# Kernel tuning notes

Hardware: AMD Instinct MI355X
Metric: run time of the kernel (lower is better)

Reference implementation:

```python
import jax, jax.numpy as jnp
import numpy as np

N_NODES = 100000
NUM_FEATURES = 512
HIDDEN = 64
NUM_CLASSES = 40
N_EDGES = 3200000
K = 10
ALPHA = 0.1


def setup_inputs() -> dict:
    key = jax.random.key(0)
    ks = jax.random.split(key, 7)
    x = jax.random.normal(ks[0], (N_NODES, NUM_FEATURES), dtype=jnp.float32)
    edge_index = jax.random.randint(ks[1], (2, N_EDGES), 0, N_NODES, dtype=jnp.int64)
    # linear layers (PyTorch Linear default init ~ U(-1/sqrt(fan_in), 1/sqrt(fan_in)))
    b1lim = 1.0 / np.sqrt(NUM_FEATURES)
    w1 = jax.random.uniform(ks[2], (NUM_FEATURES, HIDDEN), jnp.float32, -b1lim, b1lim)
    b1 = jax.random.uniform(ks[3], (HIDDEN,), jnp.float32, -b1lim, b1lim)
    b2lim = 1.0 / np.sqrt(HIDDEN)
    w2 = jax.random.uniform(ks[4], (HIDDEN, NUM_CLASSES), jnp.float32, -b2lim, b2lim)
    b2 = jax.random.uniform(ks[5], (NUM_CLASSES,), jnp.float32, -b2lim, b2lim)
    # PPR init of GPR gamma coefficients: alpha*(1-alpha)^k, last = (1-alpha)^K
    temp = ALPHA * (1.0 - ALPHA) ** np.arange(K + 1)
    temp[-1] = (1.0 - ALPHA) ** K
    temp = jnp.asarray(temp, dtype=jnp.float32)
    return {"x": x, "edge_index": edge_index, "w1": w1, "b1": b1,
            "w2": w2, "b2": b2, "temp": temp}


def reference(x, edge_index, w1, b1, w2, b2, temp):
    n = x.shape[0]
    # MLP (eval mode: dropout is identity)
    h = jax.nn.relu(x @ w1 + b1)
    h = h @ w2 + b2  # [N, C]

    gamma = jax.nn.relu(temp)

    # gcn_norm with self-loops (edge_weight = 1)
    loop = jnp.arange(n, dtype=edge_index.dtype)
    src = jnp.concatenate([edge_index[0], loop])
    dst = jnp.concatenate([edge_index[1], loop])
    ew = jnp.ones(src.shape[0], dtype=h.dtype)
    deg = jax.ops.segment_sum(ew, dst, num_segments=n)
    dinv = jnp.where(deg > 0, jax.lax.rsqrt(deg), 0.0)
    norm = dinv[src] * ew * dinv[dst]  # [E+N]

    # K-step gamma-weighted propagation: out = sum_k gamma_k * A_hat^k h
    out = gamma[0] * h
    cur = h
    for k in range(K):
        cur = jax.ops.segment_sum(norm[:, None] * cur[src], dst, num_segments=n)
        out = out + gamma[k + 1] * cur
    return jax.nn.log_softmax(out, axis=1)
```

## Files before the change

kernel.cpp:

```cpp
#include <hip/hip_runtime.h>
#include <hip/hip_bf16.h>
#include <hip/hip_fp16.h>
#include <hip/hip_fp8.h>

#define NFEAT 512
#define HID   64
#define NCLS  40

typedef short bf16x8 __attribute__((ext_vector_type(8)));
typedef float f32x4  __attribute__((ext_vector_type(4)));
typedef float v2f    __attribute__((ext_vector_type(2)));

__device__ inline short bfs(float f) {
  __hip_bfloat16 h = __float2bfloat16(f);
  return __builtin_bit_cast(short, h);
}
__device__ inline int pk(float a, float b) {
  return (int)(unsigned short)bfs(a) | ((int)(unsigned short)bfs(b) << 16);
}

__device__ inline v2f cvt2lo(int v) {
#if __has_builtin(__builtin_amdgcn_cvt_pk_f32_fp8)
  return __builtin_amdgcn_cvt_pk_f32_fp8(v, false);
#else
  v2f r; const unsigned char* b = (const unsigned char*)&v;
  __hip_fp8_e4m3 h0; h0.__x = b[0]; r[0] = (float)h0;
  __hip_fp8_e4m3 h1; h1.__x = b[1]; r[1] = (float)h1;
  return r;
#endif
}
__device__ inline v2f cvt2hi(int v) {
#if __has_builtin(__builtin_amdgcn_cvt_pk_f32_fp8)
  return __builtin_amdgcn_cvt_pk_f32_fp8(v, true);
#else
  v2f r; const unsigned char* b = (const unsigned char*)&v;
  __hip_fp8_e4m3 h0; h0.__x = b[2]; r[0] = (float)h0;
  __hip_fp8_e4m3 h1; h1.__x = b[3]; r[1] = (float)h1;
  return r;
#endif
}
__device__ inline int2 pk8f8(const float f[8]) {
#if __has_builtin(__builtin_amdgcn_cvt_pk_fp8_f32)
  int lo = 0, hi = 0;
  lo = __builtin_amdgcn_cvt_pk_fp8_f32(f[0], f[1], lo, false);
  lo = __builtin_amdgcn_cvt_pk_fp8_f32(f[2], f[3], lo, true);
  hi = __builtin_amdgcn_cvt_pk_fp8_f32(f[4], f[5], hi, false);
  hi = __builtin_amdgcn_cvt_pk_fp8_f32(f[6], f[7], hi, true);
  return make_int2(lo, hi);
#else
  int2 r; unsigned char* b = (unsigned char*)&r;
  #pragma unroll
  for (int i = 0; i < 8; ++i) { __hip_fp8_e4m3 h((float)f[i]); b[i] = h.__x; }
  return r;
#endif
}
__device__ inline unsigned char f8b(float v) {
#if __has_builtin(__builtin_amdgcn_cvt_pk_fp8_f32)
  int r = __builtin_amdgcn_cvt_pk_fp8_f32(v, v, 0, false);
  return (unsigned char)(r & 0xff);
#else
  __hip_fp8_e4m3 h(v); return h.__x;
#endif
}


static __global__ void deg_i_kernel(const int* __restrict__ dst, int* __restrict__ deg, int E) {
  int e = blockIdx.x * blockDim.x + threadIdx.x;
  if (e < E) atomicAdd(&deg[dst[e]], 1);
}

static __global__ void dinv_kernel(const int* __restrict__ deg, float* __restrict__ dinv, int N) {
  int i = blockIdx.x * blockDim.x + threadIdx.x;
  if (i < N) dinv[i] = rsqrtf((float)deg[i] + 1.0f);
}

static __global__ void w1conv_kernel(const float* __restrict__ w1, short* __restrict__ w1bf,
                                     int* __restrict__ bcnt, int nbz) {
  int t = blockIdx.x * blockDim.x + threadIdx.x;
  if (t < nbz) bcnt[t] = 0;
  if (t >= NFEAT * HID) return;
  int k = t >> 6, n = t & 63;
  w1bf[n * NFEAT + k] = bfs(w1[k * HID + n]);
}
static __global__ void w2conv_kernel(const float* __restrict__ w2, short* __restrict__ w2bf) {
  int t = blockIdx.x * blockDim.x + threadIdx.x;
  if (t >= 48 * HID) return;
  int n = t >> 6, k = t & 63;
  w2bf[t] = (n < NCLS) ? bfs(w2[k * NCLS + n]) : (short)0;
}

static __global__ __launch_bounds__(256) void mlp_mfma_kernel(
    const float* __restrict__ x, const short* __restrict__ w1bf, const float* __restrict__ b1,
    const short* __restrict__ w2bf, const float* __restrict__ b2, const float* __restrict__ temp,
    const float* __restrict__ dinv, unsigned char* __restrict__ cur, float* __restrict__ out, int N)
{
  __shared__ __align__(16) short Al[64][72];
  __shared__ __align__(16) short Bl[64][72];
  __shared__ __align__(16) short Hl[64][72];
  __shared__ __align__(16) short W2l[48][72];
  const int tid = threadIdx.x;
  const int w = tid >> 6, lane = tid & 63;
  const int q = lane >> 4, m = lane & 15;
  const long row0 = (long)blockIdx.x * 64;

  if (tid < 192) {
    int n = tid >> 2, ch = tid & 3;
    const int4* sp = (const int4*)(w2bf + n * 64 + ch * 16);
    *(int4*)&W2l[n][ch * 16]     = sp[0];
    *(int4*)&W2l[n][ch * 16 + 8] = sp[1];
  }

  f32x4 zf = {0.f, 0.f, 0.f, 0.f};
  f32x4 acc[4] = {zf, zf, zf, zf};

  const int ar = tid >> 2, ch = tid & 3;
  const long gr = row0 + ar;

  for (int kk = 0; kk < NFEAT; kk += 64) {
    float4 v0, v1, v2, v3;
    if (gr < N) {
      const float4* xp = (const float4*)(x + gr * NFEAT + kk + ch * 16);
      v0 = xp[0]; v1 = xp[1]; v2 = xp[2]; v3 = xp[3];
    } else {
      v0 = v1 = v2 = v3 = make_float4(0.f, 0.f, 0.f, 0.f);
    }
    const int4* bp = (const int4*)(w1bf + ar * NFEAT + kk + ch * 16);
    int4 bv0 = bp[0], bv1 = bp[1];

    __syncthreads();
    int4 a0 = make_int4(pk(v0.x, v0.y), pk(v0.z, v0.w), pk(v1.x, v1.y), pk(v1.z, v1.w));
    int4 a1 = make_int4(pk(v2.x, v2.y), pk(v2.z, v2.w), pk(v3.x, v3.y), pk(v3.z, v3.w));
    *(int4*)&Al[ar][ch * 16]     = a0;
    *(int4*)&Al[ar][ch * 16 + 8] = a1;
    *(int4*)&Bl[ar][ch * 16]     = bv0;
    *(int4*)&Bl[ar][ch * 16 + 8] = bv1;
    __syncthreads();

    #pragma unroll
    for (int s = 0; s < 2; ++s) {
      bf16x8 a = *(const bf16x8*)&Al[w * 16 + m][s * 32 + q * 8];
      #pragma unroll
      for (int c = 0; c < 4; ++c) {
        bf16x8 b = *(const bf16x8*)&Bl[c * 16 + m][s * 32 + q * 8];
        acc[c] = __builtin_amdgcn_mfma_f32_16x16x32_bf16(a, b, acc[c], 0, 0, 0);
      }
    }
  }

  #pragma unroll
  for (int c = 0; c < 4; ++c) {
    int col = c * 16 + m;
    float bb = b1[col];
    #pragma unroll
    for (int r = 0; r < 4; ++r) {
      int rl = w * 16 + q * 4 + r;
      Hl[rl][col] = bfs(fmaxf(acc[c][r] + bb, 0.0f));
    }
  }
  __syncthreads();

  f32x4 acc2[3] = {zf, zf, zf};
  #pragma unroll
  for (int s = 0; s < 2; ++s) {
    bf16x8 a = *(const bf16x8*)&Hl[w * 16 + m][s * 32 + q * 8];
    #pragma unroll
    for (int c = 0; c < 3; ++c) {
      bf16x8 b = *(const bf16x8*)&W2l[c * 16 + m][s * 32 + q * 8];
      acc2[c] = __builtin_amdgcn_mfma_f32_16x16x32_bf16(a, b, acc2[c], 0, 0, 0);
    }
  }

  float g0 = fmaxf(temp[0], 0.0f);
  #pragma unroll
  for (int c = 0; c < 3; ++c) {
    int col = c * 16 + m;
    if (col < NCLS) {
      float bb = b2[col];
      #pragma unroll
      for (int r = 0; r < 4; ++r) {
        long grow = row0 + w * 16 + q * 4 + r;
        if (grow < N) {
          float vv = acc2[c][r] + bb;
          cur[grow * 64 + col] = f8b(dinv[grow] * vv);
          out[grow * NCLS + col] = g0 * vv;
        }
      }
    }
  }
}


static __global__ __launch_bounds__(256) void scan1_kernel(const int* __restrict__ deg,
                                                           int* __restrict__ bsum, int N) {
  __shared__ int s[256];
  int tid = threadIdx.x;
  int i = blockIdx.x * 256 + tid;
  s[tid] = (i < N) ? deg[i] : 0;
  __syncthreads();
  for (int off = 128; off > 0; off >>= 1) {
    if (tid < off) s[tid] += s[tid + off];
    __syncthreads();
  }
  if (tid == 0) bsum[blockIdx.x] = s[0];
}

static __global__ __launch_bounds__(512) void scan2_kernel(int* __restrict__ bsum,
                                                           int* __restrict__ total, int nb) {
  __shared__ int s[512];
  int tid = threadIdx.x;
  int v = (tid < nb) ? bsum[tid] : 0;
  s[tid] = v;
  __syncthreads();
  for (int off = 1; off < 512; off <<= 1) {
    int t = (tid >= off) ? s[tid - off] : 0;
    __syncthreads();
    s[tid] += t;
    __syncthreads();
  }
  if (tid < nb) bsum[tid] = s[tid] - v;
  if (tid == 511) *total = s[511];
}

static __global__ __launch_bounds__(256) void scan3_kernel(const int* __restrict__ deg,
                                                           const int* __restrict__ bsum,
                                                           const int* __restrict__ total,
                                                           int* __restrict__ rowptr,
                                                           int* __restrict__ cursor, int N) {
  __shared__ int s[256];
  int tid = threadIdx.x;
  int i = blockIdx.x * 256 + tid;
  int v = (i < N) ? deg[i] : 0;
  s[tid] = v;
  __syncthreads();
  for (int off = 1; off < 256; off <<= 1) {
    int t = (tid >= off) ? s[tid - off] : 0;
    __syncthreads();
    s[tid] += t;
    __syncthreads();
  }
  if (i < N) {
    int e = bsum[blockIdx.x] + s[tid] - v;
    rowptr[i] = e;
    cursor[i] = e;
  }
  if (i == N) rowptr[N] = *total;
}


#define FB_EPT 16
#define FB_EPB (256 * FB_EPT)
#define FB_NBMAX 512
#define FS_CAP 12288

static __global__ __launch_bounds__(256) void bcount_kernel(
    const int* __restrict__ dst, int* __restrict__ bcnt, int E, int NB)
{
  __shared__ int cnt[FB_NBMAX];
  const int tid = threadIdx.x;
  cnt[tid] = 0; cnt[tid + 256] = 0;
  __syncthreads();
  const int e0 = blockIdx.x * FB_EPB;
  #pragma unroll
  for (int j = 0; j < FB_EPT; ++j) {
    int e = e0 + j * 256 + tid;
    if (e < E) atomicAdd(&cnt[dst[e] >> 8], 1);
  }
  __syncthreads();
  int b0 = tid, b1 = tid + 256;
  if (b0 < NB && cnt[b0]) atomicAdd(&bcnt[b0], cnt[b0]);
  if (b1 < NB && cnt[b1]) atomicAdd(&bcnt[b1], cnt[b1]);
}

static __global__ __launch_bounds__(512) void bscan_kernel(
    const int* __restrict__ bcnt, int* __restrict__ bbase, int* __restrict__ bcur,
    int* __restrict__ rowptr, int NB, int N, int E)
{
  __shared__ int s[512];
  int tid = threadIdx.x;
  int v = (tid < NB) ? bcnt[tid] : 0;
  s[tid] = v;
  __syncthreads();
  for (int off = 1; off < 512; off <<= 1) {
    int t = (tid >= off) ? s[tid - off] : 0;
    __syncthreads();
    s[tid] += t;
    __syncthreads();
  }
  if (tid < NB) { int ex = s[tid] - v; bbase[tid] = ex; bcur[tid] = ex; }
  if (tid == 0) rowptr[N] = E;
}

static __global__ __launch_bounds__(256) void fill_bin_kernel(
    const int* __restrict__ src, const int* __restrict__ dst,
    int* __restrict__ bcur, int* __restrict__ csr, int E, int NB)
{
  __shared__ int cnt[FB_NBMAX];
  __shared__ int pfx[FB_NBMAX];
  __shared__ int gbase[FB_NBMAX];
  __shared__ int stg[FB_EPB];
  __shared__ unsigned short bmap[FB_EPB];
  const int tid = threadIdx.x;
  const int e0 = blockIdx.x * FB_EPB;

  cnt[tid] = 0; cnt[tid + 256] = 0;
  __syncthreads();

  int pk_[FB_EPT], b_[FB_EPT], r_[FB_EPT];
  #pragma unroll
  for (int j = 0; j < FB_EPT; ++j) {
    int e = e0 + j * 256 + tid;
    if (e < E) {
      int s = src[e], d = dst[e];
      pk_[j] = s | ((d & 255) << 17);
      b_[j] = d >> 8;
      r_[j] = atomicAdd(&cnt[b_[j]], 1);
    } else b_[j] = -1;
  }
  __syncthreads();

  pfx[tid] = cnt[tid]; pfx[tid + 256] = cnt[tid + 256];
  __syncthreads();
  for (int off = 1; off < FB_NBMAX; off <<= 1) {
    int a = (tid >= off) ? pfx[tid - off] : 0;
    int b = (tid + 256 >= off) ? pfx[tid + 256 - off] : 0;
    __syncthreads();
    pfx[tid] += a; pfx[tid + 256] += b;
    __syncthreads();
  }

  {
    int b0 = tid, b1 = tid + 256;
    if (b0 < NB && cnt[b0]) gbase[b0] = atomicAdd(&bcur[b0], cnt[b0]);
    if (b1 < NB && cnt[b1]) gbase[b1] = atomicAdd(&bcur[b1], cnt[b1]);
  }
  __syncthreads();

  #pragma unroll
  for (int j = 0; j < FB_EPT; ++j) {
    if (b_[j] >= 0) {
      int slot = pfx[b_[j]] - cnt[b_[j]] + r_[j];
      stg[slot] = pk_[j];
      bmap[slot] = (unsigned short)b_[j];
    }
  }
  __syncthreads();

  const int total = pfx[FB_NBMAX - 1];
  for (int slot = tid; slot < total; slot += 256) {
    int b = bmap[slot];
    int local = slot - (pfx[b] - cnt[b]);
    csr[gbase[b] + local] = stg[slot];
  }
}

static __global__ __launch_bounds__(256) void fill_scatter2_kernel(
    const int* __restrict__ bbase_a, const int* __restrict__ bcnt,
    int* __restrict__ csr, const int* __restrict__ src, const int* __restrict__ dst,
    float* __restrict__ dinv, int* __restrict__ rowptr, int N, int E)
{
  __shared__ int degl[256];
  __shared__ int pfx[256];
  __shared__ int curl[256];
  __shared__ int buf[FS_CAP];
  const int tid = threadIdx.x;
  const int b = blockIdx.x;
  const int base = bbase_a[b], cnt = bcnt[b];
  const int node = (b << 8) + tid;

  degl[tid] = 0;
  __syncthreads();
  if (cnt <= FS_CAP) {
    for (int i = tid; i < cnt; i += 256) {
      int p = csr[base + i];
      atomicAdd(&degl[(p >> 17) & 255], 1);
    }
  } else {
    for (int e = tid; e < E; e += 256) {
      int d = dst[e];
      if ((d >> 8) == b) atomicAdd(&degl[d & 255], 1);
    }
  }
  __syncthreads();
  const int dv = degl[tid];
  if (node < N) dinv[node] = rsqrtf((float)dv + 1.0f);

  pfx[tid] = dv;
  __syncthreads();
  for (int off = 1; off < 256; off <<= 1) {
    int t = (tid >= off) ? pfx[tid - off] : 0;
    __syncthreads();
    pfx[tid] += t;
    __syncthreads();
  }
  const int ex = pfx[tid] - dv;
  if (node < N) rowptr[node] = base + ex;
  curl[tid] = ex;
  __syncthreads();

  if (cnt <= FS_CAP) {
    for (int i = tid; i < cnt; i += 256) {
      int p = csr[base + i];
      int ld = (p >> 17) & 255;
      int pos = atomicAdd(&curl[ld], 1);
      buf[pos] = p & 0x1FFFF;
    }
    __syncthreads();
    for (int i = tid; i < cnt; i += 256) csr[base + i] = buf[i];
  } else {
    curl[tid] = base + ex;
    __syncthreads();
    for (int e = tid; e < E; e += 256) {
      int d = dst[e];
      if ((d >> 8) == b) {
        int pos = atomicAdd(&curl[d & 255], 1);
        csr[pos] = src[e];
      }
    }
  }
}


static __global__ void fill_kernel(const int* __restrict__ src, const int* __restrict__ dst,
                                   int* __restrict__ cursor, int* __restrict__ csr, int E) {
  int e = blockIdx.x * blockDim.x + threadIdx.x;
  if (e >= E) return;
  int s = src[e], d = dst[e];
  int pos = atomicAdd(&cursor[d], 1);
  csr[pos] = s;
}


#define GR_ROWS 51
#define GR_CAP  2560

template <bool INLDS>
__device__ inline void gather_row(
    const int* __restrict__ ip, int beg, int end, unsigned c8,
    const unsigned char* __restrict__ cur,
    v2f& a0, v2f& a1, v2f& a2, v2f& a3)
{
  int e = beg;
  for (; e + 7 < end; e += 8) {
    int idx[8];
    #pragma unroll
    for (int j = 0; j < 8; ++j) idx[j] = ip[e + j];
    int2 g[8];
    #pragma unroll
    for (int j = 0; j < 8; ++j) g[j] = *(const int2*)(cur + (((unsigned)idx[j] << 6) | c8));
    #pragma unroll
    for (int j = 0; j < 8; ++j) {
      a0 += cvt2lo(g[j].x); a1 += cvt2hi(g[j].x);
      a2 += cvt2lo(g[j].y); a3 += cvt2hi(g[j].y);
    }
  }
  for (; e + 3 < end; e += 4) {
    int idx[4];
    #pragma unroll
    for (int j = 0; j < 4; ++j) idx[j] = ip[e + j];
    int2 g[4];
    #pragma unroll
    for (int j = 0; j < 4; ++j) g[j] = *(const int2*)(cur + (((unsigned)idx[j] << 6) | c8));
    #pragma unroll
    for (int j = 0; j < 4; ++j) {
      a0 += cvt2lo(g[j].x); a1 += cvt2hi(g[j].x);
      a2 += cvt2lo(g[j].y); a3 += cvt2hi(g[j].y);
    }
  }
  for (; e < end; ++e) {
    int2 g = *(const int2*)(cur + (((unsigned)ip[e] << 6) | c8));
    a0 += cvt2lo(g.x); a1 += cvt2hi(g.x);
    a2 += cvt2lo(g.y); a3 += cvt2hi(g.y);
  }
}

static __global__ __launch_bounds__(256) void gather_kernel(
    const int* __restrict__ rowptr, const int* __restrict__ csr,
    const float* __restrict__ dinv, const float* __restrict__ temp, int k,
    const unsigned char* __restrict__ cur, unsigned char* __restrict__ nxt,
    float4* __restrict__ out, int N)
{
  __shared__ int rp[GR_ROWS + 1];
  __shared__ int lidx[GR_CAP];
  const int tid = threadIdx.x;
  const int row0 = blockIdx.x * GR_ROWS;
  const int nrows = min(GR_ROWS, N - row0);

  if (tid <= nrows) rp[tid] = rowptr[row0 + tid];
  __syncthreads();
  const int beg0 = rp[0];
  const int count = rp[nrows] - beg0;
  const bool inlds = (count <= GR_CAP);
  if (inlds) {
    for (int i = tid; i < count; i += 256) lidx[i] = csr[beg0 + i];
  }
  __syncthreads();

  const int r = tid / 5, c4 = tid - r * 5;
  if (r >= nrows) return;
  const int row = row0 + r;
  const unsigned c8 = (unsigned)c4 * 8;
  const float dv = dinv[row];

  v2f a0, a1, a2, a3;
  {
    int2 v = *(const int2*)(cur + (((unsigned)row << 6) | c8));
    a0 = cvt2lo(v.x); a1 = cvt2hi(v.x);
    a2 = cvt2lo(v.y); a3 = cvt2hi(v.y);
  }

  if (inlds) {
    gather_row<true>(lidx, rp[r] - beg0, rp[r + 1] - beg0, c8, cur, a0, a1, a2, a3);
  } else {
    gather_row<false>(csr, rp[r], rp[r + 1], c8, cur, a0, a1, a2, a3);
  }

  float d2 = dv * dv;
  float y[8] = {d2 * a0[0], d2 * a0[1], d2 * a1[0], d2 * a1[1],
                d2 * a2[0], d2 * a2[1], d2 * a3[0], d2 * a3[1]};
  *(int2*)(nxt + (((unsigned)row << 6) | c8)) = pk8f8(y);

  float gd = fmaxf(temp[k], 0.0f) * dv;
  int oi = row * 10 + c4 * 2;
  float4 o0 = out[oi], o1 = out[oi + 1];
  out[oi]     = make_float4(fmaf(gd, a0[0], o0.x), fmaf(gd, a0[1], o0.y),
                            fmaf(gd, a1[0], o0.z), fmaf(gd, a1[1], o0.w));
  out[oi + 1] = make_float4(fmaf(gd, a2[0], o1.x), fmaf(gd, a2[1], o1.y),
                            fmaf(gd, a3[0], o1.z), fmaf(gd, a3[1], o1.w));
}


static __global__ void selfloop_kernel(const float* __restrict__ dinv, const float4* __restrict__ cur,
                                       float4* __restrict__ nxt, int n10) {
  int t = blockIdx.x * blockDim.x + threadIdx.x;
  if (t >= n10) return;
  int i = t / 10;
  float dv = dinv[i], s = dv * dv;
  float4 v = cur[t];
  nxt[t] = make_float4(s * v.x, s * v.y, s * v.z, s * v.w);
}

static __global__ void scatter_kernel(const int* __restrict__ src, const int* __restrict__ dst,
                                      const float* __restrict__ dinv,
                                      const float4* __restrict__ cur, float* __restrict__ nxt, int items) {
  int t = blockIdx.x * blockDim.x + threadIdx.x;
  if (t >= items) return;
  int e = t / 10, c4 = t - e * 10;
  int s = src[e], d = dst[e];
  float nm = dinv[s] * dinv[d];
  float4 v = cur[s * 10 + c4];
  float* np = nxt + (size_t)d * NCLS + c4 * 4;
  unsafeAtomicAdd(np + 0, nm * v.x);
  unsafeAtomicAdd(np + 1, nm * v.y);
  unsafeAtomicAdd(np + 2, nm * v.z);
  unsafeAtomicAdd(np + 3, nm * v.w);
}

static __global__ void axpy_kernel(const float* __restrict__ temp, int k,
                                   const float4* __restrict__ nxt, float4* __restrict__ out, int n10) {
  int t = blockIdx.x * blockDim.x + threadIdx.x;
  if (t >= n10) return;
  float g = fmaxf(temp[k], 0.0f);
  float4 v = nxt[t], o = out[t];
  out[t] = make_float4(o.x + g * v.x, o.y + g * v.y, o.z + g * v.z, o.w + g * v.w);
}

static __global__ __launch_bounds__(256) void mlp_kernel(
    const float* __restrict__ x, const float* __restrict__ w1, const float* __restrict__ b1,
    const float* __restrict__ w2, const float* __restrict__ b2, const float* __restrict__ temp,
    float* __restrict__ cur, float* __restrict__ out, int N)
{
  __shared__ __align__(16) float xs[4][NFEAT];
  __shared__ float hs[4][HID];
  const int w = threadIdx.x >> 6, lane = threadIdx.x & 63;
  const int i = blockIdx.x * 4 + w;
  if (i < N) {
    const float4* xrow = (const float4*)(x + (size_t)i * NFEAT);
    float4* xsr = (float4*)xs[w];
    xsr[lane]      = xrow[lane];
    xsr[lane + 64] = xrow[lane + 64];
  }
  __syncthreads();
  if (i < N) {
    float acc = b1[lane];
    #pragma unroll 8
    for (int k = 0; k < NFEAT; ++k)
      acc = fmaf(xs[w][k], w1[k * HID + lane], acc);
    hs[w][lane] = fmaxf(acc, 0.0f);
  }
  __syncthreads();
  if (i < N && lane < NCLS) {
    float a2 = b2[lane];
    #pragma unroll
    for (int j = 0; j < HID; ++j)
      a2 = fmaf(hs[w][j], w2[j * NCLS + lane], a2);
    float g0 = fmaxf(temp[0], 0.0f);
    cur[(size_t)i * NCLS + lane] = a2;
    out[(size_t)i * NCLS + lane] = g0 * a2;
  }
}

static __global__ void logsoftmax_kernel(float* __restrict__ out, int N) {
  int i = blockIdx.x * blockDim.x + threadIdx.x;
  if (i >= N) return;
  float4* row = (float4*)(out + (size_t)i * NCLS);
  float4 v[10];
  float m = -3.4e38f;
  #pragma unroll
  for (int r = 0; r < 10; ++r) {
    v[r] = row[r];
    m = fmaxf(m, fmaxf(fmaxf(v[r].x, v[r].y), fmaxf(v[r].z, v[r].w)));
  }
  float sum = 0.0f;
  #pragma unroll
  for (int r = 0; r < 10; ++r)
    sum += __expf(v[r].x - m) + __expf(v[r].y - m) + __expf(v[r].z - m) + __expf(v[r].w - m);
  float l = m + __logf(sum);
  #pragma unroll
  for (int r = 0; r < 10; ++r)
    row[r] = make_float4(v[r].x - l, v[r].y - l, v[r].z - l, v[r].w - l);
}


extern "C" void kernel_launch(void* const* d_in, const int* in_sizes, int n_in,
                              void* d_out, int out_size, void* d_ws, size_t ws_size,
                              hipStream_t stream) {
  const float* x    = (const float*)d_in[0];
  const int*   ei   = (const int*)d_in[1];
  const float* w1   = (const float*)d_in[2];
  const float* b1   = (const float*)d_in[3];
  const float* w2   = (const float*)d_in[4];
  const float* b2   = (const float*)d_in[5];
  const float* temp = (const float*)d_in[6];

  const int N = in_sizes[0] / NFEAT;
  const int E = in_sizes[1] / 2;
  const int* src = ei;
  const int* dst = ei + E;
  float* out = (float*)d_out;

  char* ws = (char*)d_ws;
  size_t off = 0;
  auto alloc = [&](size_t bytes) { size_t o = off; off += (bytes + 255) & ~(size_t)255; return o; };
  float* dinv   = (float*)(ws + alloc((size_t)N * 4));
  int*   deg    = (int*)  (ws + alloc((size_t)N * 4));
  unsigned char* curA = (unsigned char*)(ws + alloc((size_t)N * 64));
  unsigned char* curB = (unsigned char*)(ws + alloc((size_t)N * 64));
  int*   rowptr = (int*)  (ws + alloc((size_t)(N + 1) * 4));
  int*   cursor = (int*)  (ws + alloc((size_t)N * 4));
  int*   bsum   = (int*)  (ws + alloc(1024 * 4));
  int*   total  = (int*)  (ws + alloc(256));
  int*   bcnt   = (int*)  (ws + alloc(FB_NBMAX * 4));
  int*   bbase  = (int*)  (ws + alloc(FB_NBMAX * 4));
  int*   bcur   = (int*)  (ws + alloc(FB_NBMAX * 4));
  short* w1bf   = (short*)(ws + alloc((size_t)NFEAT * HID * 2));
  short* w2bf   = (short*)(ws + alloc((size_t)48 * HID * 2));
  int*   csr    = (int*)  (ws + alloc((size_t)E * 4));
  float* fA     = (float*)curA;
  const bool csr_ok = (off <= ws_size);

  const int NB = (N + 255) >> 8;
  const int gblocks = (N + GR_ROWS - 1) / GR_ROWS;

  if (csr_ok && NB <= FB_NBMAX && N <= (1 << 17)) {
    w1conv_kernel<<<(NFEAT * HID + 255) / 256, 256, 0, stream>>>(w1, w1bf, bcnt, FB_NBMAX);
    w2conv_kernel<<<(48 * HID + 255) / 256, 256, 0, stream>>>(w2, w2bf);

    bcount_kernel<<<(E + FB_EPB - 1) / FB_EPB, 256, 0, stream>>>(dst, bcnt, E, NB);
    bscan_kernel<<<1, 512, 0, stream>>>(bcnt, bbase, bcur, rowptr, NB, N, E);
    fill_bin_kernel<<<(E + FB_EPB - 1) / FB_EPB, 256, 0, stream>>>(src, dst, bcur, csr, E, NB);
    fill_scatter2_kernel<<<NB, 256, 0, stream>>>(bbase, bcnt, csr, src, dst, dinv, rowptr, N, E);

    mlp_mfma_kernel<<<(N + 63) / 64, 256, 0, stream>>>(x, w1bf, b1, w2bf, b2, temp, dinv,
                                                       curA, out, N);

    unsigned char* cur = curA;
    unsigned char* nxt = curB;
    for (int k = 0; k < 10; ++k) {
      gather_kernel<<<gblocks, 256, 0, stream>>>(
          rowptr, csr, dinv, temp, k + 1, cur, nxt, (float4*)out, N);
      unsigned char* t2 = cur; cur = nxt; nxt = t2;
    }
    logsoftmax_kernel<<<(N + 255) / 256, 256, 0, stream>>>(out, N);
    return;
  }

  (void)hipMemsetAsync(deg, 0, (size_t)N * sizeof(int), stream);
  deg_i_kernel<<<(E + 255) / 256, 256, 0, stream>>>(dst, deg, E);
  dinv_kernel<<<(N + 255) / 256, 256, 0, stream>>>(deg, dinv, N);

  if (csr_ok) {
    w1conv_kernel<<<(NFEAT * HID + 255) / 256, 256, 0, stream>>>(w1, w1bf, bcnt, FB_NBMAX);
    w2conv_kernel<<<(48 * HID + 255) / 256, 256, 0, stream>>>(w2, w2bf);
    mlp_mfma_kernel<<<(N + 63) / 64, 256, 0, stream>>>(x, w1bf, b1, w2bf, b2, temp, dinv,
                                                       curA, out, N);

    const int nb = (N + 255) / 256;
    scan1_kernel<<<nb, 256, 0, stream>>>(deg, bsum, N);
    scan2_kernel<<<1, 512, 0, stream>>>(bsum, total, nb);
    scan3_kernel<<<(N + 256) / 256, 256, 0, stream>>>(deg, bsum, total, rowptr, cursor, N);
    fill_kernel<<<(E + 255) / 256, 256, 0, stream>>>(src, dst, cursor, csr, E);

    unsigned char* cur = curA;
    unsigned char* nxt = curB;
    for (int k = 0; k < 10; ++k) {
      gather_kernel<<<gblocks, 256, 0, stream>>>(
          rowptr, csr, dinv, temp, k + 1, cur, nxt, (float4*)out, N);
      unsigned char* t2 = cur; cur = nxt; nxt = t2;
    }
  } else {
    float* fB = (float*)curB;
    mlp_kernel<<<(N + 3) / 4, 256, 0, stream>>>(x, w1, b1, w2, b2, temp, fA, out, N);
    const int n10 = N * 10;
    const int items = E * 10;
    float* cur = fA;
    float* nxt = fB;
    for (int k = 0; k < 10; ++k) {
      selfloop_kernel<<<(n10 + 255) / 256, 256, 0, stream>>>(dinv, (const float4*)cur, (float4*)nxt, n10);
      scatter_kernel<<<(items + 255) / 256, 256, 0, stream>>>(src, dst, dinv, (const float4*)cur, nxt, items);
      axpy_kernel<<<(n10 + 255) / 256, 256, 0, stream>>>(temp, k + 1, (const float4*)nxt, (float4*)out, n10);
      float* t2 = cur; cur = nxt; nxt = t2;
    }
  }

  logsoftmax_kernel<<<(N + 255) / 256, 256, 0, stream>>>(out, N);
}
```

Baseline: 763.1 us.

## Archive per-hop propagation results and fuse gamma accumulation into final log-softmax

Each gather hop now writes its scaled result to a separate archive slice with nontemporal stores instead of read-modify-writing the output accumulator. A new final kernel reads all ten archived hops, applies the gamma weights, and computes log-softmax in one pass. CSR index loads in the gather also become nontemporal. This removes the per-hop read of the output buffer, but it needs a large extra workspace (N*40*10 floats) and the final kernel still reads all of it, so total traffic may not fall. If the larger workspace no longer fits, csr_ok can fail and force the slow fallback path.

```diff
diff --git a/kernel.cpp b/kernel.cpp
--- a/kernel.cpp
+++ b/kernel.cpp
@@ -17,6 +17,13 @@
 }
 __device__ inline int pk(float a, float b) {
   return (int)(unsigned short)bfs(a) | ((int)(unsigned short)bfs(b) << 16);
+}
+
+__device__ inline f32x4 ntl4(const float4* p) {
+  return __builtin_nontemporal_load((const f32x4*)p);
+}
+__device__ inline void nts4(float4* p, f32x4 v) {
+  __builtin_nontemporal_store(v, (f32x4*)p);
 }
 
 __device__ inline v2f cvt2lo(int v) {
@@ -475,9 +482,9 @@
 
 static __global__ __launch_bounds__(256) void gather_kernel(
     const int* __restrict__ rowptr, const int* __restrict__ csr,
-    const float* __restrict__ dinv, const float* __restrict__ temp, int k,
+    const float* __restrict__ dinv,
     const unsigned char* __restrict__ cur, unsigned char* __restrict__ nxt,
-    float4* __restrict__ out, int N)
+    float4* __restrict__ arch, int N)
 {
   __shared__ int rp[GR_ROWS + 1];
   __shared__ int lidx[GR_CAP];
@@ -491,7 +498,8 @@
   const int count = rp[nrows] - beg0;
   const bool inlds = (count <= GR_CAP);
   if (inlds) {
-    for (int i = tid; i < count; i += 256) lidx[i] = csr[beg0 + i];
+    for (int i = tid; i < count; i += 256)
+      lidx[i] = __builtin_nontemporal_load(csr + beg0 + i);
   }
   __syncthreads();
 
@@ -519,13 +527,42 @@
                 d2 * a2[0], d2 * a2[1], d2 * a3[0], d2 * a3[1]};
   *(int2*)(nxt + (((unsigned)row << 6) | c8)) = pk8f8(y);
 
-  float gd = fmaxf(temp[k], 0.0f) * dv;
+  f32x4 v0 = {dv * a0[0], dv * a0[1], dv * a1[0], dv * a1[1]};
+  f32x4 v1 = {dv * a2[0], dv * a2[1], dv * a3[0], dv * a3[1]};
   int oi = row * 10 + c4 * 2;
-  float4 o0 = out[oi], o1 = out[oi + 1];
-  out[oi]     = make_float4(fmaf(gd, a0[0], o0.x), fmaf(gd, a0[1], o0.y),
-                            fmaf(gd, a1[0], o0.z), fmaf(gd, a1[1], o0.w));
-  out[oi + 1] = make_float4(fmaf(gd, a2[0], o1.x), fmaf(gd, a2[1], o1.y),
-                            fmaf(gd, a3[0], o1.z), fmaf(gd, a3[1], o1.w));
+  nts4(&arch[oi], v0);
+  nts4(&arch[oi + 1], v1);
+}
+
+static __global__ void finsm_kernel(float* __restrict__ out, const float4* __restrict__ arch,
+                                    const float* __restrict__ temp, int N) {
+  int i = blockIdx.x * blockDim.x + threadIdx.x;
+  if (i >= N) return;
+  float4* row = (float4*)(out + (size_t)i * NCLS);
+  f32x4 v[10];
+  #pragma unroll
+  for (int r = 0; r < 10; ++r) { float4 t = row[r]; v[r] = f32x4{t.x, t.y, t.z, t.w}; }
+  for (int k = 0; k < 10; ++k) {
+    float g = fmaxf(temp[k + 1], 0.0f);
+    const float4* ar = arch + (size_t)k * N * 10 + (size_t)i * 10;
+    #pragma unroll
+    for (int r = 0; r < 10; ++r) {
+      f32x4 a = ntl4(ar + r);
+      v[r] += g * a;
+    }
+  }
+  float m = -3.4e38f;
+  #pragma unroll
+  for (int r = 0; r < 10; ++r)
+    m = fmaxf(m, fmaxf(fmaxf(v[r][0], v[r][1]), fmaxf(v[r][2], v[r][3])));
+  float sum = 0.0f;
+  #pragma unroll
+  for (int r = 0; r < 10; ++r)
+    sum += __expf(v[r][0] - m) + __expf(v[r][1] - m) + __expf(v[r][2] - m) + __expf(v[r][3] - m);
+  float l = m + __logf(sum);
+  #pragma unroll
+  for (int r = 0; r < 10; ++r)
+    row[r] = make_float4(v[r][0] - l, v[r][1] - l, v[r][2] - l, v[r][3] - l);
 }
 
 
@@ -655,6 +692,7 @@
   short* w1bf   = (short*)(ws + alloc((size_t)NFEAT * HID * 2));
   short* w2bf   = (short*)(ws + alloc((size_t)48 * HID * 2));
   int*   csr    = (int*)  (ws + alloc((size_t)E * 4));
+  float4* arch  = (float4*)(ws + alloc((size_t)N * 40 * 4 * 10));
   float* fA     = (float*)curA;
   const bool csr_ok = (off <= ws_size);
 
@@ -677,10 +715,10 @@
     unsigned char* nxt = curB;
     for (int k = 0; k < 10; ++k) {
       gather_kernel<<<gblocks, 256, 0, stream>>>(
-          rowptr, csr, dinv, temp, k + 1, cur, nxt, (float4*)out, N);
+          rowptr, csr, dinv, cur, nxt, arch + (size_t)k * N * 10, N);
       unsigned char* t2 = cur; cur = nxt; nxt = t2;
     }
-    logsoftmax_kernel<<<(N + 255) / 256, 256, 0, stream>>>(out, N);
+    finsm_kernel<<<(N + 255) / 256, 256, 0, stream>>>(out, arch, temp, N);
     return;
   }
 
@@ -704,9 +742,10 @@
     unsigned char* nxt = curB;
     for (int k = 0; k < 10; ++k) {
       gather_kernel<<<gblocks, 256, 0, stream>>>(
-          rowptr, csr, dinv, temp, k + 1, cur, nxt, (float4*)out, N);
+          rowptr, csr, dinv, cur, nxt, arch + (size_t)k * N * 10, N);
       unsigned char* t2 = cur; cur = nxt; nxt = t2;
     }
+    finsm_kernel<<<(N + 255) / 256, 256, 0, stream>>>(out, arch, temp, N);
   } else {
     float* fB = (float*)curB;
     mlp_kernel<<<(N + 3) / 4, 256, 0, stream>>>(x, w1, b1, w2, b2, temp, fA, out, N);
@@ -720,7 +759,6 @@
       axpy_kernel<<<(n10 + 255) / 256, 256, 0, stream>>>(temp, k + 1, (const float4*)nxt, (float4*)out, n10);
       float* t2 = cur; cur = nxt; nxt = t2;
     }
-  }
-
-  logsoftmax_kernel<<<(N + 255) / 256, 256, 0, stream>>>(out, N);
-}
+    logsoftmax_kernel<<<(N + 255) / 256, 256, 0, stream>>>(out, N);
+  }
+}
```

New measurement: 889.1 us. 1.17x slower.
